# Kernel optimization log

Hardware: AMD Instinct MI355X
Metric: run time of the kernel (lower is better)

Reference implementation:

```python
import jax, jax.numpy as jnp
import numpy as np

B, N, H, F = 256, 256, 256, 64   # batch, nodes, hidden, output
NNB = 4                          # neighbors per node (nns - 1)
HEADS = 3
S = 2 ** NNB - 1                 # nonempty subsets for Mobius Choquet
# MASK[s, i] = True iff neighbor i is in subset s (subsets 1..2^n-1)
MASK = jnp.asarray(np.array([[(s >> i) & 1 for i in range(NNB)] for s in range(1, S + 1)], dtype=bool))


def setup_inputs() -> dict:
    key = jax.random.key(0)
    ks = jax.random.split(key, 12)
    w = 0.02
    centers = jnp.arange(N, dtype=jnp.int64)[:, None]
    neigh = jax.random.randint(ks[11], (N, NNB), 0, N).astype(jnp.int64)
    local_edges = jnp.concatenate([centers, neigh], axis=1)[:, None, :]  # [N, 1, 5]
    return {
        "observation": jax.random.normal(ks[0], (B, N, H), jnp.float32),
        "action": jax.random.normal(ks[1], (B, N, H), jnp.float32),
        "V_W1": jax.random.normal(ks[2], (N, H, H), jnp.float32) * w,
        "V_b1": jnp.zeros((N, H), jnp.float32),
        "V_W2": jax.random.normal(ks[3], (N, H, F), jnp.float32) * w,
        "V_b2": jnp.zeros((N, F), jnp.float32),
        "A_W1": jax.random.normal(ks[4], (N, 2 * H, H), jnp.float32) * w,
        "A_b1": jnp.zeros((N, H), jnp.float32),
        "A_W2": jax.random.normal(ks[5], (N, H, F), jnp.float32) * w,
        "A_b2": jnp.zeros((N, F), jnp.float32),
        "chi_m": jax.random.normal(ks[6], (N, HEADS, S), jnp.float32) * w,
        "local_edges": local_edges,
    }


def _mmlp2(x, W1, b1, W2, b2):
    # per-node (multi) 2-layer MLP: first layer ReLU, second linear (act=False)
    h = jax.nn.relu(jnp.einsum('bni,nio->bno', x, W1) + b1)
    return jnp.einsum('bnh,nho->bno', h, W2) + b2


def reference(observation, action, V_W1, V_b1, V_W2, V_b2,
              A_W1, A_b1, A_W2, A_b2, chi_m, local_edges):
    V = _mmlp2(observation, V_W1, V_b1, V_W2, V_b2)                      # [B,N,F]
    A = _mmlp2(jnp.concatenate([observation, action], axis=-1),
               A_W1, A_b1, A_W2, A_b2)                                   # [B,N,F]
    Q = A + V                                                            # [B,N,F]
    centers = local_edges[:, 0, 0]        # [N]
    neigh = local_edges[:, 0, 1:]         # [N, NNB]
    # .data in torch -> detach the gathered neighbor Q-values
    Qn = jax.lax.stop_gradient(Q[:, neigh, :])                           # [B,N,NNB,F]
    # Mobius Choquet: min over each nonempty subset of neighbors
    masked = jnp.where(MASK[None, None, :, :, None], Qn[:, :, None, :, :], jnp.inf)
    mins = masked.min(axis=3)                                            # [B,N,S,F]
    chi = jnp.einsum('bnsf,nhs->bnf', mins, chi_m) / HEADS               # [B,N,F]
    return (chi + Q[:, centers, :]).mean(axis=-1)                        # [B,N]
```

## Files before the change

kernel.cpp:

```cpp
#include <hip/hip_runtime.h>
#include <cstddef>


#define BN 256
#define HD 256
#define FD 64
#define XS 40
#define SLS 268

typedef _Float16 f16x8 __attribute__((ext_vector_type(8)));
typedef _Float16 f16x4 __attribute__((ext_vector_type(4)));
typedef float f32x4 __attribute__((ext_vector_type(4)));

#define GLOAD16(g, l)                                              \
  __builtin_amdgcn_global_load_lds(                                \
      (__attribute__((address_space(1))) void*)(g),                \
      (__attribute__((address_space(3))) void*)(l), 16, 0, 0)

#define WAIT_BAR(VMCNT_STR)                                        \
  asm volatile("s_waitcnt " VMCNT_STR " lgkmcnt(0)" ::: "memory"); \
  __builtin_amdgcn_s_barrier();                                    \
  asm volatile("" ::: "memory");

__device__ __forceinline__ void x_load(const float* xs0, const float* xs1, int n,
                                       int kt, int tid, float4 xr[4]) {
  int kOff = kt * 32;
  const float* xs = (kOff < 256) ? xs0 : xs1;
  int l = tid & 63, w = tid >> 6;
  const float* base = xs + (size_t)n * HD + (kOff & 255) + (l & 7) * 4;
#pragma unroll
  for (int i = 0; i < 4; ++i) {
    int row = w * 32 + i * 8 + (l >> 3);
    xr[i] = *(const float4*)(base + (size_t)row * (BN * HD));
  }
}
__device__ __forceinline__ void x_write(_Float16* Xl, int tid, const float4 xr[4]) {
  int l = tid & 63, w = tid >> 6;
#pragma unroll
  for (int i = 0; i < 4; ++i) {
    int row = w * 32 + i * 8 + (l >> 3);
    f16x4 v;
    v[0] = (_Float16)xr[i].x; v[1] = (_Float16)xr[i].y;
    v[2] = (_Float16)xr[i].z; v[3] = (_Float16)xr[i].w;
    *(f16x4*)(Xl + row * XS + (l & 7) * 4) = v;
  }
}

__device__ __forceinline__ void w1_gload(const float* __restrict__ Wg, float* Wl,
                                         int ktile, int w, int lane) {
#pragma unroll
  for (int s = 0; s < 4; ++s) {
    int rl = w * 4 + s;
    int swz = ((rl >> 3) & 3) << 4;
    const float* src = Wg + (size_t)(ktile * 32 + rl) * HD + ((lane * 4) ^ swz);
    GLOAD16(src, Wl + rl * HD);
  }
}

__device__ __forceinline__ void w2_gload_half(const float* __restrict__ W2g, float* chunk,
                                              int half, int w, int lane) {
#pragma unroll
  for (int s = 0; s < 4; ++s) {
    int rl = (w * 4 + s) * 4;
    int swz = ((rl >> 3) & 3) << 4;
    const float* src = W2g + (size_t)(half * 128 + rl + (lane >> 4)) * FD
                       + (((lane & 15) * 4) ^ swz);
    GLOAD16(src, chunk + rl * FD);
  }
}

__device__ __forceinline__ void g1_compute(const float* Wc, const _Float16* Xc,
                                           int lrow, int lq, int Nbase, int wm1,
                                           f32x4 acc[8][4]) {
  int lk8 = lq * 8;
  const float* wbase = Wc + lk8 * 256;
  f16x8 b[4];
#pragma unroll
  for (int nf = 0; nf < 4; ++nf) {
    int col = (Nbase + nf * 16 + lrow) ^ (lq << 4);
    f16x8 t;
#pragma unroll
    for (int j = 0; j < 8; ++j) t[j] = (_Float16)wbase[j * 256 + col];
    b[nf] = t;
  }
#pragma unroll
  for (int m = 0; m < 8; ++m) {
    f16x8 a = *(const f16x8*)(Xc + (wm1 * 128 + m * 16 + lrow) * XS + lk8);
#pragma unroll
    for (int nf = 0; nf < 4; ++nf)
      acc[m][nf] = __builtin_amdgcn_mfma_f32_16x16x32_f16(a, b[nf], acc[m][nf], 0, 0, 0);
  }
}

template <int NK>
__device__ __forceinline__ void run_gemm1(const float* xs0, const float* xs1,
                                          const float* __restrict__ Wg,
                                          const float* __restrict__ W2g,
                                          int n, int tid, int lrow, int lq,
                                          int Nbase, int wm1, int w, int lane,
                                          float* Wring, _Float16* Xl0, _Float16* Xl1,
                                          f32x4 acc[8][4]) {
  float* w0 = Wring;
  float* w1 = Wring + 8192;
  float* w2 = Wring + 16384;
  float4 xrA[4], xrB[4];
  x_load(xs0, xs1, n, 0, tid, xrA);
  w1_gload(Wg, w0, 0, w, lane);
  x_load(xs0, xs1, n, 1, tid, xrB);
  w1_gload(Wg, w1, 1, w, lane);
  x_write(Xl0, tid, xrA);
  WAIT_BAR("vmcnt(8)")
#pragma unroll 1
  for (int kt = 0; kt < NK; kt += 2) {
    if (kt + 2 < NK) {
      x_load(xs0, xs1, n, kt + 2, tid, xrA);
      w1_gload(Wg, w2, kt + 2, w, lane);
    } else {
      w2_gload_half(W2g, w2, 0, w, lane);
    }
    g1_compute(w0, Xl0, lrow, lq, Nbase, wm1, acc);
    if (kt + 1 < NK) x_write(Xl1, tid, xrB);
    if (kt < NK - 2) { WAIT_BAR("vmcnt(8)") }
    else             { WAIT_BAR("vmcnt(4)") }
    { float* t = w0; w0 = w1; w1 = w2; w2 = t; }
    if (kt + 3 < NK) {
      x_load(xs0, xs1, n, kt + 3, tid, xrB);
      w1_gload(Wg, w2, kt + 3, w, lane);
    } else {
      w2_gload_half(W2g, w2, 1, w, lane);
    }
    g1_compute(w0, Xl1, lrow, lq, Nbase, wm1, acc);
    if (kt + 2 < NK) {
      x_write(Xl0, tid, xrA);
      WAIT_BAR("vmcnt(8)")
    }
    { float* t = w0; w0 = w1; w1 = w2; w2 = t; }
  }
}

__device__ __forceinline__ void gemm2_branch(f32x4 acc[8][4], f32x4 acc2[2][4],
                                             const float* cA, const float* cB,
                                             const float* __restrict__ b1g,
                                             _Float16* slab, int lrow, int lq,
                                             int Nbase, int wm1, int wn1, int w) {
  int lk8 = lq * 8;
  float bv[4];
#pragma unroll
  for (int nf = 0; nf < 4; ++nf) bv[nf] = b1g[Nbase + nf * 16 + lrow];
#pragma unroll 1
  for (int s = 0; s < 4; ++s) {
    if (wn1 == s) {
#pragma unroll
      for (int m = 0; m < 8; ++m)
#pragma unroll
        for (int nf = 0; nf < 4; ++nf) {
          f16x4 hv;
#pragma unroll
          for (int r = 0; r < 4; ++r)
            hv[r] = (_Float16)fmaxf(acc[m][nf][r] + bv[nf], 0.f);
          *(f16x4*)(slab + (nf * 16 + lrow) * SLS + wm1 * 128 + m * 16 + lq * 4) = hv;
        }
    }
    __syncthreads();
#pragma unroll
    for (int kf = 0; kf < 2; ++kf) {
      const int r0 = s * 64 + kf * 32;
      const float* wb2 = ((r0 < 128) ? cA : cB) + ((r0 & 127) + lk8) * FD;
      f16x8 a2[2], bb[4];
#pragma unroll
      for (int mf = 0; mf < 2; ++mf) {
        f16x8 t;
#pragma unroll
        for (int j = 0; j < 8; ++j)
          t[j] = slab[(kf * 32 + lk8 + j) * SLS + w * 32 + mf * 16 + lrow];
        a2[mf] = t;
      }
#pragma unroll
      for (int nf = 0; nf < 4; ++nf) {
        int col = (nf * 16 + lrow) ^ (lq << 4);
        f16x8 t;
#pragma unroll
        for (int j = 0; j < 8; ++j) t[j] = (_Float16)wb2[j * FD + col];
        bb[nf] = t;
      }
#pragma unroll
      for (int mf = 0; mf < 2; ++mf)
#pragma unroll
        for (int nf = 0; nf < 4; ++nf)
          acc2[mf][nf] =
              __builtin_amdgcn_mfma_f32_16x16x32_f16(a2[mf], bb[nf], acc2[mf][nf], 0, 0, 0);
    }
    __syncthreads();
  }
}

__global__ __launch_bounds__(512, 2) void phase1_kernel(
    const float* __restrict__ obs, const float* __restrict__ act,
    const float* __restrict__ V_W1, const float* __restrict__ V_b1,
    const float* __restrict__ V_W2, const float* __restrict__ V_b2,
    const float* __restrict__ A_W1, const float* __restrict__ A_b1,
    const float* __restrict__ A_W2, const float* __restrict__ A_b2,
    float* __restrict__ Q) {
  __shared__ __align__(16) float smem[34816];
  float* Wring = smem;
  _Float16* Xl0 = (_Float16*)(smem + 24576);
  _Float16* Xl1 = Xl0 + 10240;
  _Float16* slab = (_Float16*)(smem + 24576);

  int tid = threadIdx.x;
  int l = tid & 63, w = tid >> 6, lane = l;
  int lrow = l & 15, lq = l >> 4;
  int wm1 = w >> 2, wn1 = w & 3;
  int Nbase = wn1 * 64;
  int n = blockIdx.x;

  f32x4 acc[8][4];
  f32x4 acc2[2][4];
#pragma unroll
  for (int i = 0; i < 2; ++i)
#pragma unroll
    for (int j = 0; j < 4; ++j) acc2[i][j] = (f32x4){0.f, 0.f, 0.f, 0.f};

#pragma unroll
  for (int m = 0; m < 8; ++m)
#pragma unroll
    for (int nf = 0; nf < 4; ++nf) acc[m][nf] = (f32x4){0.f, 0.f, 0.f, 0.f};
  run_gemm1<8>(obs, obs, V_W1 + (size_t)n * HD * HD, V_W2 + (size_t)n * HD * FD,
               n, tid, lrow, lq, Nbase, wm1, w, lane, Wring, Xl0, Xl1, acc);
  __syncthreads();
  gemm2_branch(acc, acc2, Wring + 16384 , Wring ,
               V_b1 + n * HD, slab, lrow, lq, Nbase, wm1, wn1, w);

#pragma unroll
  for (int m = 0; m < 8; ++m)
#pragma unroll
    for (int nf = 0; nf < 4; ++nf) acc[m][nf] = (f32x4){0.f, 0.f, 0.f, 0.f};
  run_gemm1<16>(obs, act, A_W1 + (size_t)n * 2 * HD * HD, A_W2 + (size_t)n * HD * FD,
                n, tid, lrow, lq, Nbase, wm1, w, lane, Wring, Xl0, Xl1, acc);
  __syncthreads();
  gemm2_branch(acc, acc2, Wring + 8192 , Wring + 16384 ,
               A_b1 + n * HD, slab, lrow, lq, Nbase, wm1, wn1, w);

  const float* vb2 = V_b2 + n * FD;
  const float* ab2 = A_b2 + n * FD;
#pragma unroll
  for (int mf = 0; mf < 2; ++mf)
#pragma unroll
    for (int nf = 0; nf < 4; ++nf) {
      int f = nf * 16 + lrow;
      float bias = vb2[f] + ab2[f];
#pragma unroll
      for (int rr = 0; rr < 4; ++rr) {
        int row = w * 32 + mf * 16 + lq * 4 + rr;
        Q[(size_t)row * (BN * FD) + n * FD + f] = acc2[mf][nf][rr] + bias;
      }
    }
}

__global__ __launch_bounds__(256) void phase2_kernel(const float* __restrict__ Q,
                                                     const float* __restrict__ chi_m,
                                                     const int* __restrict__ le,
                                                     float* __restrict__ out) {
  int b = blockIdx.x;
  int n = threadIdx.x;
  int step = (le[5] == 1) ? 1 : 2;
  const int* e = le + n * 5 * step;
  int c  = e[0 * step] & (BN - 1);
  int n0 = e[1 * step] & (BN - 1);
  int n1 = e[2 * step] & (BN - 1);
  int n2 = e[3 * step] & (BN - 1);
  int n3 = e[4 * step] & (BN - 1);
  const float* ch = chi_m + n * 45;
  float cm[15];
#pragma unroll
  for (int s = 0; s < 15; ++s) cm[s] = (ch[s] + ch[15 + s] + ch[30 + s]) * (1.f / 3.f);
  const float* qb = Q + (size_t)b * (BN * FD);
  const float* q0 = qb + n0 * FD;
  const float* q1 = qb + n1 * FD;
  const float* q2 = qb + n2 * FD;
  const float* q3 = qb + n3 * FD;
  const float* qc = qb + c * FD;
  float acc = 0.f;
#pragma unroll
  for (int f = 0; f < FD; f += 4) {
    float4 v0 = *(const float4*)(q0 + f);
    float4 v1 = *(const float4*)(q1 + f);
    float4 v2 = *(const float4*)(q2 + f);
    float4 v3 = *(const float4*)(q3 + f);
    float4 vc = *(const float4*)(qc + f);
    const float* p0 = (const float*)&v0;
    const float* p1 = (const float*)&v1;
    const float* p2 = (const float*)&v2;
    const float* p3 = (const float*)&v3;
    const float* pc = (const float*)&vc;
#pragma unroll
    for (int u = 0; u < 4; ++u) {
      float a = p0[u], bq = p1[u], cq = p2[u], d = p3[u];
      float m01 = fminf(a, bq), m02 = fminf(a, cq), m03 = fminf(a, d);
      float m12 = fminf(bq, cq), m13 = fminf(bq, d), m23 = fminf(cq, d);
      float m012 = fminf(m01, cq), m013 = fminf(m01, d);
      float m023 = fminf(m02, d),  m123 = fminf(m12, d);
      float m0123 = fminf(m01, m23);
      float chi = cm[0] * a   + cm[1] * bq   + cm[2] * m01  + cm[3] * cq
                + cm[4] * m02 + cm[5] * m12  + cm[6] * m012 + cm[7] * d
                + cm[8] * m03 + cm[9] * m13  + cm[10] * m013 + cm[11] * m23
                + cm[12] * m023 + cm[13] * m123 + cm[14] * m0123;
      acc += chi + pc[u];
    }
  }
  out[b * BN + n] = acc * (1.f / 64.f);
}

extern "C" void kernel_launch(void* const* d_in, const int* in_sizes, int n_in,
                              void* d_out, int out_size, void* d_ws, size_t ws_size,
                              hipStream_t stream) {
  (void)in_sizes; (void)n_in; (void)out_size; (void)ws_size;
  const float* obs  = (const float*)d_in[0];
  const float* act  = (const float*)d_in[1];
  const float* V_W1 = (const float*)d_in[2];
  const float* V_b1 = (const float*)d_in[3];
  const float* V_W2 = (const float*)d_in[4];
  const float* V_b2 = (const float*)d_in[5];
  const float* A_W1 = (const float*)d_in[6];
  const float* A_b1 = (const float*)d_in[7];
  const float* A_W2 = (const float*)d_in[8];
  const float* A_b2 = (const float*)d_in[9];
  const float* chim = (const float*)d_in[10];
  const int*   le   = (const int*)d_in[11];
  float* Q   = (float*)d_ws;
  float* out = (float*)d_out;

  phase1_kernel<<<dim3(256), dim3(512), 0, stream>>>(obs, act, V_W1, V_b1, V_W2, V_b2,
                                                     A_W1, A_b1, A_W2, A_b2, Q);
  phase2_kernel<<<dim3(256), dim3(256), 0, stream>>>(Q, chim, le, out);
}
```

Measured before the change: 116.5 us.

## Deepen weight prefetch to a four-slot ring with single X buffer

Replaces the three-slot weight ring and double-buffered X tile in the first-layer GEMM with a four-slot weight ring (three tiles in flight) and a single X tile in LDS. The loop now processes one k-tile per iteration, with a barrier before overwriting X and a waitcnt allowing 12 outstanding loads. This aims to hide more global-memory latency on the weight stream. In exchange it uses more LDS (about 148KB per block, which may cut occupancy from two blocks per CU) and adds an extra barrier per k-step.

```diff
diff --git a/kernel.cpp b/kernel.cpp
--- a/kernel.cpp
+++ b/kernel.cpp
@@ -17,9 +17,13 @@
       (__attribute__((address_space(1))) void*)(g),                \
       (__attribute__((address_space(3))) void*)(l), 16, 0, 0)
 
-#define WAIT_BAR(VMCNT_STR)                                        \
-  asm volatile("s_waitcnt " VMCNT_STR " lgkmcnt(0)" ::: "memory"); \
-  __builtin_amdgcn_s_barrier();                                    \
+#define WAIT_BAR12()                                                       \
+  asm volatile("s_waitcnt vmcnt(12) lgkmcnt(0)" ::: "memory");             \
+  __builtin_amdgcn_s_barrier();                                            \
+  asm volatile("" ::: "memory");
+#define BAR_LGKM()                                                         \
+  asm volatile("s_waitcnt lgkmcnt(0)" ::: "memory");                       \
+  __builtin_amdgcn_s_barrier();                                            \
   asm volatile("" ::: "memory");
 
 __device__ __forceinline__ void x_load(const float* xs0, const float* xs1, int n,
@@ -98,43 +102,34 @@
                                           const float* __restrict__ W2g,
                                           int n, int tid, int lrow, int lq,
                                           int Nbase, int wm1, int w, int lane,
-                                          float* Wring, _Float16* Xl0, _Float16* Xl1,
+                                          float* ring, _Float16* Xl,
                                           f32x4 acc[8][4]) {
-  float* w0 = Wring;
-  float* w1 = Wring + 8192;
-  float* w2 = Wring + 16384;
   float4 xrA[4], xrB[4];
   x_load(xs0, xs1, n, 0, tid, xrA);
-  w1_gload(Wg, w0, 0, w, lane);
+  w1_gload(Wg, ring, 0, w, lane);
   x_load(xs0, xs1, n, 1, tid, xrB);
-  w1_gload(Wg, w1, 1, w, lane);
-  x_write(Xl0, tid, xrA);
-  WAIT_BAR("vmcnt(8)")
+  w1_gload(Wg, ring + 8192, 1, w, lane);
+  w1_gload(Wg, ring + 16384, 2, w, lane);
+  x_write(Xl, tid, xrA);
+  WAIT_BAR12()
 #pragma unroll 1
-  for (int kt = 0; kt < NK; kt += 2) {
-    if (kt + 2 < NK) {
-      x_load(xs0, xs1, n, kt + 2, tid, xrA);
-      w1_gload(Wg, w2, kt + 2, w, lane);
-    } else {
-      w2_gload_half(W2g, w2, 0, w, lane);
-    }
-    g1_compute(w0, Xl0, lrow, lq, Nbase, wm1, acc);
-    if (kt + 1 < NK) x_write(Xl1, tid, xrB);
-    if (kt < NK - 2) { WAIT_BAR("vmcnt(8)") }
-    else             { WAIT_BAR("vmcnt(4)") }
-    { float* t = w0; w0 = w1; w1 = w2; w2 = t; }
+  for (int kt = 0; kt < NK; ++kt) {
+    float* slot = ring + (size_t)(kt & 3) * 8192;
     if (kt + 3 < NK) {
-      x_load(xs0, xs1, n, kt + 3, tid, xrB);
-      w1_gload(Wg, w2, kt + 3, w, lane);
-    } else {
-      w2_gload_half(W2g, w2, 1, w, lane);
-    }
-    g1_compute(w0, Xl1, lrow, lq, Nbase, wm1, acc);
-    if (kt + 2 < NK) {
-      x_write(Xl0, tid, xrA);
-      WAIT_BAR("vmcnt(8)")
-    }
-    { float* t = w0; w0 = w1; w1 = w2; w2 = t; }
+      x_load(xs0, xs1, n, kt + 2, tid, (kt & 1) ? xrB : xrA);
+      w1_gload(Wg, ring + (size_t)((kt + 3) & 3) * 8192, kt + 3, w, lane);
+    } else if (kt + 3 == NK) {
+      x_load(xs0, xs1, n, kt + 2, tid, (kt & 1) ? xrB : xrA);
+      w2_gload_half(W2g, ring + (size_t)(NK & 3) * 8192, 0, w, lane);
+    } else if (kt + 3 == NK + 1) {
+      w2_gload_half(W2g, ring + (size_t)((NK + 1) & 3) * 8192, 1, w, lane);
+    }
+    g1_compute(slot, Xl, lrow, lq, Nbase, wm1, acc);
+    if (kt + 1 < NK) {
+      BAR_LGKM()
+      x_write(Xl, tid, (kt & 1) ? xrA : xrB);
+      WAIT_BAR12()
+    }
   }
 }
 
@@ -201,11 +196,10 @@
     const float* __restrict__ A_W1, const float* __restrict__ A_b1,
     const float* __restrict__ A_W2, const float* __restrict__ A_b2,
     float* __restrict__ Q) {
-  __shared__ __align__(16) float smem[34816];
-  float* Wring = smem;
-  _Float16* Xl0 = (_Float16*)(smem + 24576);
-  _Float16* Xl1 = Xl0 + 10240;
-  _Float16* slab = (_Float16*)(smem + 24576);
+  __shared__ __align__(16) float smem[37888];
+  float* ring = smem;
+  _Float16* Xl = (_Float16*)(smem + 32768);
+  _Float16* slab = (_Float16*)(smem + 16384);
 
   int tid = threadIdx.x;
   int l = tid & 63, w = tid >> 6, lane = l;
@@ -226,9 +220,9 @@
 #pragma unroll
     for (int nf = 0; nf < 4; ++nf) acc[m][nf] = (f32x4){0.f, 0.f, 0.f, 0.f};
   run_gemm1<8>(obs, obs, V_W1 + (size_t)n * HD * HD, V_W2 + (size_t)n * HD * FD,
-               n, tid, lrow, lq, Nbase, wm1, w, lane, Wring, Xl0, Xl1, acc);
+               n, tid, lrow, lq, Nbase, wm1, w, lane, ring, Xl, acc);
   __syncthreads();
-  gemm2_branch(acc, acc2, Wring + 16384 , Wring ,
+  gemm2_branch(acc, acc2, ring , ring + 8192 ,
                V_b1 + n * HD, slab, lrow, lq, Nbase, wm1, wn1, w);
 
 #pragma unroll
@@ -236,9 +230,9 @@
 #pragma unroll
     for (int nf = 0; nf < 4; ++nf) acc[m][nf] = (f32x4){0.f, 0.f, 0.f, 0.f};
   run_gemm1<16>(obs, act, A_W1 + (size_t)n * 2 * HD * HD, A_W2 + (size_t)n * HD * FD,
-                n, tid, lrow, lq, Nbase, wm1, w, lane, Wring, Xl0, Xl1, acc);
+                n, tid, lrow, lq, Nbase, wm1, w, lane, ring, Xl, acc);
   __syncthreads();
-  gemm2_branch(acc, acc2, Wring + 8192 , Wring + 16384 ,
+  gemm2_branch(acc, acc2, ring , ring + 8192 ,
                A_b1 + n * HD, slab, lrow, lq, Nbase, wm1, wn1, w);
 
   const float* vb2 = V_b2 + n * FD;
```

Measured after the change: 169.1 us. 45.1% more time.
